# Kernel tuning notes

Hardware: AMD Instinct MI355X
Metric: run time of the kernel (lower is better)

## Reference

```python
import jax, jax.numpy as jnp
import numpy as np

K = 32  # neighbors per point (self.k)

def setup_inputs() -> dict:
    key = jax.random.key(0)
    k1, k2 = jax.random.split(key)
    B, N, C = 16, 4096, 64
    x = jax.random.normal(k1, (B, N, C), dtype=jnp.float32)
    idx = jax.random.randint(k2, (B, N, K), 0, N, dtype=jnp.int64)
    return {"x": x, "idx": idx}

def reference(x, idx):
    # pooled[b, n, :] = mean_k x[b, idx[b, n, k], :]
    # gather per-batch: xb[ib] -> [N, K, C]
    gathered = jax.vmap(lambda xb, ib: xb[ib])(x, idx)  # [B, N, K, C]
    return gathered.mean(axis=2)  # [B, N, C]
```

## Files before the change

### kernel.cpp

```cpp
#include <hip/hip_runtime.h>


#define BB 16
#define NN 4096
#define KK 32
#define CC 64
#define CH8 8
#define NCHUNK (CC / CH8)
#define NQ 4
#define PTS (NN / NQ)
#define THREADS 512

__device__ __forceinline__ uint pk_bf16(float a, float b) {
    uint ua = __float_as_uint(a);
    ua = (ua + 0x7fffu + ((ua >> 16) & 1u)) >> 16;
    uint ub = __float_as_uint(b);
    ub = (ub + 0x7fffu + ((ub >> 16) & 1u)) & 0xffff0000u;
    return ua | ub;
}

__device__ __forceinline__ void acc8(float a[8], uint4 r) {
    a[0] += __uint_as_float(r.x << 16);
    a[1] += __uint_as_float(r.x & 0xffff0000u);
    a[2] += __uint_as_float(r.y << 16);
    a[3] += __uint_as_float(r.y & 0xffff0000u);
    a[4] += __uint_as_float(r.z << 16);
    a[5] += __uint_as_float(r.z & 0xffff0000u);
    a[6] += __uint_as_float(r.w << 16);
    a[7] += __uint_as_float(r.w & 0xffff0000u);
}

__global__ __launch_bounds__(THREADS, 4)
void gapool_fused(const float* __restrict__ x,
                  const int* __restrict__ idx32,
                  float* __restrict__ out) {
    __shared__ uint4 tile[NN];

    const int bid = blockIdx.x;
    const int b = bid & 15;
    const int g = bid >> 4;
    const int chunk = g & (NCHUNK - 1);
    const int q = g >> 3;
    const int tid = threadIdx.x;
    const float s = 1.0f / KK;

    int vprobe = idx32[2 * (tid & 63) + 1];
    const bool is64 = (__ballot(vprobe != 0) == 0ULL);

    {
        const float4* __restrict__ x4 =
            (const float4*)x + (size_t)b * NN * (CC / 4) + chunk * 2;
#pragma unroll
        for (int i = 0; i < NN / THREADS; ++i) {
            const int r = i * THREADS + tid;
            const float4 v0 = x4[(size_t)r * (CC / 4)];
            const float4 v1 = x4[(size_t)r * (CC / 4) + 1];
            tile[r] = make_uint4(pk_bf16(v0.x, v0.y), pk_bf16(v0.z, v0.w),
                                 pk_bf16(v1.x, v1.y), pk_bf16(v1.z, v1.w));
        }
    }
    __syncthreads();

    const size_t pbase = (size_t)b * NN + (size_t)q * PTS;
    float* __restrict__ outq = out + pbase * CC + chunk * CH8;

    if (is64) {
        const uint4* __restrict__ ib = (const uint4*)idx32 + pbase * (KK / 2);
#pragma unroll
        for (int pp = 0; pp < PTS / THREADS; ++pp) {
            const int p = pp * THREADS + tid;
            const uint4* __restrict__ ip = ib + (size_t)p * (KK / 2);
            float a[8] = {0.f, 0.f, 0.f, 0.f, 0.f, 0.f, 0.f, 0.f};
#pragma unroll
            for (int t = 0; t < KK / 2; ++t) {
                const uint4 w = ip[t];
                acc8(a, tile[w.x]);
                acc8(a, tile[w.z]);
            }
            float4* op = (float4*)(outq + (size_t)p * CC);
            op[0] = make_float4(a[0] * s, a[1] * s, a[2] * s, a[3] * s);
            op[1] = make_float4(a[4] * s, a[5] * s, a[6] * s, a[7] * s);
        }
    } else {
        const uint4* __restrict__ ib = (const uint4*)idx32 + pbase * (KK / 4);
#pragma unroll
        for (int pp = 0; pp < PTS / THREADS; ++pp) {
            const int p = pp * THREADS + tid;
            const uint4* __restrict__ ip = ib + (size_t)p * (KK / 4);
            float a[8] = {0.f, 0.f, 0.f, 0.f, 0.f, 0.f, 0.f, 0.f};
#pragma unroll
            for (int t = 0; t < KK / 4; ++t) {
                const uint4 w = ip[t];
                acc8(a, tile[w.x]);
                acc8(a, tile[w.y]);
                acc8(a, tile[w.z]);
                acc8(a, tile[w.w]);
            }
            float4* op = (float4*)(outq + (size_t)p * CC);
            op[0] = make_float4(a[0] * s, a[1] * s, a[2] * s, a[3] * s);
            op[1] = make_float4(a[4] * s, a[5] * s, a[6] * s, a[7] * s);
        }
    }
}

extern "C" void kernel_launch(void* const* d_in, const int* in_sizes, int n_in,
                              void* d_out, int out_size, void* d_ws, size_t ws_size,
                              hipStream_t stream) {
    const float* x     = (const float*)d_in[0];
    const int*   idx32 = (const int*)d_in[1];
    float*       out   = (float*)d_out;
    (void)d_ws; (void)ws_size;

    gapool_fused<<<BB * NCHUNK * NQ, THREADS, 0, stream>>>(x, idx32, out);
}
```

Measured before the change: 91.33 us.

## Split bf16 conversion into prep kernel and gather rows directly from global memory

Replaces the per-block LDS tile of a channel chunk with a separate prep kernel that writes a bf16 copy of x to workspace, followed by a gather kernel where 8 lanes cooperate on one point, each owning 8 channels and fetching full 128-byte rows. Neighbor indices are loaded once per point and distributed via shuffles instead of being re-read for every channel chunk. This removes repeated index reads and LDS staging, at the cost of an extra launch and cache-dependent random global gathers.

Result: faster. 86.08 us (-5.7%).

```diff
diff --git a/kernel.cpp b/kernel.cpp
--- a/kernel.cpp
+++ b/kernel.cpp
@@ -5,11 +5,10 @@
 #define NN 4096
 #define KK 32
 #define CC 64
-#define CH8 8
-#define NCHUNK (CC / CH8)
-#define NQ 4
-#define PTS (NN / NQ)
-#define THREADS 512
+#define THREADS 256
+#define MAIN_BLOCKS (BB * NN * 8 / THREADS)
+#define PREP_BLOCKS 2048
+#define PREP_THREADS 256
 
 __device__ __forceinline__ uint pk_bf16(float a, float b) {
     uint ua = __float_as_uint(a);
@@ -19,88 +18,64 @@
     return ua | ub;
 }
 
-__device__ __forceinline__ void acc8(float a[8], uint4 r) {
-    a[0] += __uint_as_float(r.x << 16);
-    a[1] += __uint_as_float(r.x & 0xffff0000u);
-    a[2] += __uint_as_float(r.y << 16);
-    a[3] += __uint_as_float(r.y & 0xffff0000u);
-    a[4] += __uint_as_float(r.z << 16);
-    a[5] += __uint_as_float(r.z & 0xffff0000u);
-    a[6] += __uint_as_float(r.w << 16);
-    a[7] += __uint_as_float(r.w & 0xffff0000u);
+__global__ __launch_bounds__(PREP_THREADS)
+void prep_kernel(const float4* __restrict__ x4, uint4* __restrict__ xb) {
+    const int u = blockIdx.x * PREP_THREADS + threadIdx.x;
+    const float4 v0 = x4[2 * (size_t)u];
+    const float4 v1 = x4[2 * (size_t)u + 1];
+    xb[u] = make_uint4(pk_bf16(v0.x, v0.y), pk_bf16(v0.z, v0.w),
+                       pk_bf16(v1.x, v1.y), pk_bf16(v1.z, v1.w));
 }
 
-__global__ __launch_bounds__(THREADS, 4)
-void gapool_fused(const float* __restrict__ x,
-                  const int* __restrict__ idx32,
-                  float* __restrict__ out) {
-    __shared__ uint4 tile[NN];
-
+__global__ __launch_bounds__(THREADS)
+void gapool_gather(const uint4* __restrict__ xb,
+                   const int* __restrict__ idx32,
+                   float* __restrict__ out) {
     const int bid = blockIdx.x;
     const int b = bid & 15;
-    const int g = bid >> 4;
-    const int chunk = g & (NCHUNK - 1);
-    const int q = g >> 3;
+    const int seg = bid >> 4;
     const int tid = threadIdx.x;
+    const int cl = tid & 7;
+    const int p = seg * (THREADS / 8) + (tid >> 3);
     const float s = 1.0f / KK;
 
     int vprobe = idx32[2 * (tid & 63) + 1];
     const bool is64 = (__ballot(vprobe != 0) == 0ULL);
 
-    {
-        const float4* __restrict__ x4 =
-            (const float4*)x + (size_t)b * NN * (CC / 4) + chunk * 2;
+    const size_t prow = (size_t)b * NN + p;
+
+    uint pre0, pre1, pre2, pre3;
+    if (is64) {
+        const uint4* ip = (const uint4*)idx32 + prow * (KK * 2 / 4) + cl * 2;
+        const uint4 A = ip[0], B = ip[1];
+        pre0 = A.x; pre1 = A.z; pre2 = B.x; pre3 = B.z;
+    } else {
+        const uint4 A = ((const uint4*)idx32)[prow * (KK / 4) + cl];
+        pre0 = A.x; pre1 = A.y; pre2 = A.z; pre3 = A.w;
+    }
+
+    const uint4* __restrict__ xbb = xb + (size_t)b * NN * (CC / 8);
+
+    float a[8] = {0.f, 0.f, 0.f, 0.f, 0.f, 0.f, 0.f, 0.f};
 #pragma unroll
-        for (int i = 0; i < NN / THREADS; ++i) {
-            const int r = i * THREADS + tid;
-            const float4 v0 = x4[(size_t)r * (CC / 4)];
-            const float4 v1 = x4[(size_t)r * (CC / 4) + 1];
-            tile[r] = make_uint4(pk_bf16(v0.x, v0.y), pk_bf16(v0.z, v0.w),
-                                 pk_bf16(v1.x, v1.y), pk_bf16(v1.z, v1.w));
-        }
+    for (int t = 0; t < KK; ++t) {
+        const uint pj = (t & 3) == 0 ? pre0 : (t & 3) == 1 ? pre1
+                      : (t & 3) == 2 ? pre2 : pre3;
+        const uint nb = __shfl(pj, t >> 2, 8);
+        const uint4 r = xbb[(size_t)nb * (CC / 8) + cl];
+        a[0] += __uint_as_float(r.x << 16);
+        a[1] += __uint_as_float(r.x & 0xffff0000u);
+        a[2] += __uint_as_float(r.y << 16);
+        a[3] += __uint_as_float(r.y & 0xffff0000u);
+        a[4] += __uint_as_float(r.z << 16);
+        a[5] += __uint_as_float(r.z & 0xffff0000u);
+        a[6] += __uint_as_float(r.w << 16);
+        a[7] += __uint_as_float(r.w & 0xffff0000u);
     }
-    __syncthreads();
 
-    const size_t pbase = (size_t)b * NN + (size_t)q * PTS;
-    float* __restrict__ outq = out + pbase * CC + chunk * CH8;
-
-    if (is64) {
-        const uint4* __restrict__ ib = (const uint4*)idx32 + pbase * (KK / 2);
-#pragma unroll
-        for (int pp = 0; pp < PTS / THREADS; ++pp) {
-            const int p = pp * THREADS + tid;
-            const uint4* __restrict__ ip = ib + (size_t)p * (KK / 2);
-            float a[8] = {0.f, 0.f, 0.f, 0.f, 0.f, 0.f, 0.f, 0.f};
-#pragma unroll
-            for (int t = 0; t < KK / 2; ++t) {
-                const uint4 w = ip[t];
-                acc8(a, tile[w.x]);
-                acc8(a, tile[w.z]);
-            }
-            float4* op = (float4*)(outq + (size_t)p * CC);
-            op[0] = make_float4(a[0] * s, a[1] * s, a[2] * s, a[3] * s);
-            op[1] = make_float4(a[4] * s, a[5] * s, a[6] * s, a[7] * s);
-        }
-    } else {
-        const uint4* __restrict__ ib = (const uint4*)idx32 + pbase * (KK / 4);
-#pragma unroll
-        for (int pp = 0; pp < PTS / THREADS; ++pp) {
-            const int p = pp * THREADS + tid;
-            const uint4* __restrict__ ip = ib + (size_t)p * (KK / 4);
-            float a[8] = {0.f, 0.f, 0.f, 0.f, 0.f, 0.f, 0.f, 0.f};
-#pragma unroll
-            for (int t = 0; t < KK / 4; ++t) {
-                const uint4 w = ip[t];
-                acc8(a, tile[w.x]);
-                acc8(a, tile[w.y]);
-                acc8(a, tile[w.z]);
-                acc8(a, tile[w.w]);
-            }
-            float4* op = (float4*)(outq + (size_t)p * CC);
-            op[0] = make_float4(a[0] * s, a[1] * s, a[2] * s, a[3] * s);
-            op[1] = make_float4(a[4] * s, a[5] * s, a[6] * s, a[7] * s);
-        }
-    }
+    float4* op = (float4*)(out + prow * CC + cl * 8);
+    op[0] = make_float4(a[0] * s, a[1] * s, a[2] * s, a[3] * s);
+    op[1] = make_float4(a[4] * s, a[5] * s, a[6] * s, a[7] * s);
 }
 
 extern "C" void kernel_launch(void* const* d_in, const int* in_sizes, int n_in,
@@ -109,7 +84,9 @@
     const float* x     = (const float*)d_in[0];
     const int*   idx32 = (const int*)d_in[1];
     float*       out   = (float*)d_out;
-    (void)d_ws; (void)ws_size;
+    uint4*       xb    = (uint4*)d_ws;
 
-    gapool_fused<<<BB * NCHUNK * NQ, THREADS, 0, stream>>>(x, idx32, out);
+    prep_kernel<<<PREP_BLOCKS, PREP_THREADS, 0, stream>>>((const float4*)x, xb);
+
+    gapool_gather<<<MAIN_BLOCKS, THREADS, 0, stream>>>(xb, idx32, out);
 }
```
